# Kernel optimization log

Measured on AMD Instinct MI355X. Metric: run time of the kernel, lower is better.

The kernel has to match this reference:

```python
import jax, jax.numpy as jnp
import numpy as np

P, T, UNITS = 256, 65536, 128
WIDTH = 1.0


def setup_inputs() -> dict:
    key = jax.random.key(0)
    k1, k2, k3 = jax.random.split(key, 3)
    inputs = jax.random.normal(k1, (P, T), dtype=jnp.float32)
    player_weights = jax.random.normal(k2, (P,), dtype=jnp.float32)
    kernel = jax.random.normal(k3, (T, UNITS), dtype=jnp.float32) * 0.01
    bias = jnp.zeros((UNITS,), dtype=jnp.float32)
    state = jnp.zeros((P,), dtype=jnp.float32)
    return {"inputs": inputs, "player_weights": player_weights,
            "kernel": kernel, "bias": bias, "state": state}


def _phi(x):
    # Phi(x) = max(x,0) + min(x+width,0)
    return jnp.maximum(x, 0.0) + jnp.minimum(x + WIDTH, 0.0)


def _play_scan(x_seq, s0):
    # sequential play-operator recurrence: s_t = Phi(w*x_t - s_{t-1}) + s_{t-1}
    def step(s, x):
        s_new = _phi(x - s) + s
        return s_new, s_new
    _, ys = jax.lax.scan(step, s0, x_seq)
    return ys  # [T]


def reference(inputs, player_weights, kernel, bias, state):
    scaled = inputs * player_weights[:, None]          # [P, T]
    outs = jax.vmap(_play_scan)(scaled, state)         # [P, T]
    y = outs @ kernel + bias                           # [P, units]
    return jnp.tanh(y)
```

## Files before the change

### kernel.cpp

```cpp
#include <hip/hip_runtime.h>
#include <math.h>

#define Pn 256
#define Tn 65536
#define Un 128
#define NC 256
#define CHUNK 256
#define ST 32

typedef float f4 __attribute__((ext_vector_type(4)));

__global__ __launch_bounds__(1024) void kA(const float* __restrict__ in,
                                           const float* __restrict__ pw,
                                           float* __restrict__ Aarr,
                                           float* __restrict__ Barr) {
  __shared__ float As[4][Pn], Bs[4][Pn];
  const int c = blockIdx.x, tid = threadIdx.x;
  const int q = tid >> 8, p = tid & 255;
  const float w = pw[p];
  const f4* src = (const f4*)(in + (size_t)p * Tn + c * CHUNK + q * 64);
  float A = -3.402823466e38f, B = 3.402823466e38f;
#pragma unroll
  for (int i = 0; i < 16; ++i) {
    f4 v = src[i];
#pragma unroll
    for (int j = 0; j < 4; ++j) {
      float x = v[j] * w;
      A = fmaxf(A, x);
      B = fminf(fmaxf(B, x), x + 1.0f);
    }
  }
  As[q][p] = A;
  Bs[q][p] = B;
  __syncthreads();
  if (tid < Pn) {
    float Ac = As[0][tid], Bc = Bs[0][tid];
#pragma unroll
    for (int qq = 1; qq < 4; ++qq) {
      float a2 = As[qq][tid], b2 = Bs[qq][tid];
      Bc = fminf(fmaxf(Bc, a2), b2);
      Ac = fmaxf(Ac, a2);
    }
    Aarr[c * Pn + tid] = Ac;
    Barr[c * Pn + tid] = Bc;
  }
}

__global__ __launch_bounds__(256) void kB(const float* __restrict__ Aarr,
                                          const float* __restrict__ Barr,
                                          const float* __restrict__ st,
                                          float* __restrict__ sinb) {
  const int p = threadIdx.x;
  float s = st[p];
  for (int c = 0; c < NC; ++c) {
    sinb[c * Pn + p] = s;
    s = fminf(fmaxf(s, Aarr[c * Pn + p]), Barr[c * Pn + p]);
  }
}

template <bool ATOMIC>
__global__ __launch_bounds__(256, 1) void kC(const float* __restrict__ in,
                                             const float* __restrict__ pw,
                                             const float* __restrict__ Kg,
                                             const float* __restrict__ sinb,
                                             float* __restrict__ outp) {
  __shared__ float sS[ST][Pn];
  __shared__ float sK[ST][Un];
  const int c = blockIdx.x, tid = threadIdx.x;

  const float w = pw[tid];
  float s = sinb[c * Pn + tid];
  const f4* src = (const f4*)(in + (size_t)tid * Tn + c * CHUNK);

  const int ug = tid & 7, pg = tid >> 3;
  const int p0 = pg * 8;
  float acc[8][16];
#pragma unroll
  for (int a = 0; a < 8; ++a)
#pragma unroll
    for (int b = 0; b < 16; ++b) acc[a][b] = 0.0f;

  const f4* Kt = (const f4*)(Kg + (size_t)c * CHUNK * Un);

  for (int sub = 0; sub < CHUNK / ST; ++sub) {
#pragma unroll
    for (int k = 0; k < 4; ++k) {
      int idx = k * 256 + tid;
      int r = idx >> 5, col = idx & 31;
      *(f4*)&sK[r][col * 4] = Kt[(size_t)(sub * ST + r) * (Un / 4) + col];
    }
#pragma unroll
    for (int i4 = 0; i4 < ST / 4; ++i4) {
      f4 v = src[sub * (ST / 4) + i4];
#pragma unroll
      for (int j = 0; j < 4; ++j) {
        float x = v[j] * w;
        s = fminf(fmaxf(s, x), x + 1.0f);
        sS[i4 * 4 + j][tid] = s;
      }
    }
    __syncthreads();
#pragma unroll 2
    for (int i = 0; i < ST; ++i) {
      f4 sv0 = *(const f4*)&sS[i][p0];
      f4 sv1 = *(const f4*)&sS[i][p0 + 4];
      f4 kv0 = *(const f4*)&sK[i][ug * 4];
      f4 kv1 = *(const f4*)&sK[i][32 + ug * 4];
      f4 kv2 = *(const f4*)&sK[i][64 + ug * 4];
      f4 kv3 = *(const f4*)&sK[i][96 + ug * 4];
#pragma unroll
      for (int a = 0; a < 8; ++a) {
        float sa = (a < 4) ? sv0[a] : sv1[a - 4];
#pragma unroll
        for (int l = 0; l < 4; ++l) {
          acc[a][0 + l]  += sa * kv0[l];
          acc[a][4 + l]  += sa * kv1[l];
          acc[a][8 + l]  += sa * kv2[l];
          acc[a][12 + l] += sa * kv3[l];
        }
      }
    }
    __syncthreads();
  }

  if (ATOMIC) {
#pragma unroll
    for (int a = 0; a < 8; ++a)
#pragma unroll
      for (int k = 0; k < 4; ++k)
#pragma unroll
        for (int l = 0; l < 4; ++l)
          atomicAdd(&outp[(size_t)(p0 + a) * Un + k * 32 + ug * 4 + l],
                    acc[a][k * 4 + l]);
  } else {
    float* base = outp + (size_t)c * (Pn * Un);
#pragma unroll
    for (int a = 0; a < 8; ++a)
#pragma unroll
      for (int k = 0; k < 4; ++k) {
        f4 v;
#pragma unroll
        for (int l = 0; l < 4; ++l) v[l] = acc[a][k * 4 + l];
        *(f4*)&base[(size_t)(p0 + a) * Un + k * 32 + ug * 4] = v;
      }
  }
}

__global__ __launch_bounds__(256) void kD(const float* __restrict__ part,
                                          const float* __restrict__ bias,
                                          float* __restrict__ out) {
  const int g = blockIdx.x * 256 + threadIdx.x;
  const int u = g & (Un - 1);
  float a = 0.0f;
#pragma unroll 8
  for (int c = 0; c < NC; ++c) a += part[(size_t)c * (Pn * Un) + g];
  out[g] = tanhf(a + bias[u]);
}

__global__ __launch_bounds__(256) void kD2(float* __restrict__ out,
                                           const float* __restrict__ bias) {
  const int g = blockIdx.x * 256 + threadIdx.x;
  out[g] = tanhf(out[g] + bias[g & (Un - 1)]);
}

extern "C" void kernel_launch(void* const* d_in, const int* in_sizes, int n_in,
                              void* d_out, int out_size, void* d_ws,
                              size_t ws_size, hipStream_t stream) {
  const float* in   = (const float*)d_in[0];
  const float* pw   = (const float*)d_in[1];
  const float* Kg   = (const float*)d_in[2];
  const float* bias = (const float*)d_in[3];
  const float* st   = (const float*)d_in[4];
  float* out = (float*)d_out;
  float* ws = (float*)d_ws;

  float* Aarr = ws;
  float* Barr = ws + NC * Pn;
  float* sinb = ws + 2 * NC * Pn;
  float* part = ws + 262144;

  const size_t needPart =
      (262144 + (size_t)NC * Pn * Un) * sizeof(float);

  kA<<<NC, 1024, 0, stream>>>(in, pw, Aarr, Barr);
  kB<<<1, Pn, 0, stream>>>(Aarr, Barr, st, sinb);

  if (ws_size >= needPart) {
    kC<false><<<NC, 256, 0, stream>>>(in, pw, Kg, sinb, part);
    kD<<<(Pn * Un) / 256, 256, 0, stream>>>(part, bias, out);
  } else {
    hipMemsetAsync(d_out, 0, (size_t)Pn * Un * sizeof(float), stream);
    kC<true><<<NC, 256, 0, stream>>>(in, pw, Kg, sinb, out);
    kD2<<<(Pn * Un) / 256, 256, 0, stream>>>(out, bias);
  }
}
```

Measured before the change: 231.5 us.

## Halve chunk size, wave-reduce clamp summaries, parallelize carry scan, widen GEMM blocks

Chunks are cut from 256 to 128 steps, giving 512 chunks. kA now reduces each chunk's clamp summary with wave shuffles, one wave per (player, chunk). kB scans the carries in two levels using 1024 threads instead of one serial 256-thread loop. kC uses 512-thread blocks with a 4x2 by 4x2 register tile, where only half the threads run the recurrence. kD splits its partial sum over four thread groups. The aim is more parallelism and shorter serial chains, but it doubles the partial-sum buffer that kD must read.

```diff
diff --git a/kernel.cpp b/kernel.cpp
--- a/kernel.cpp
+++ b/kernel.cpp
@@ -4,119 +4,139 @@
 #define Pn 256
 #define Tn 65536
 #define Un 128
-#define NC 256
-#define CHUNK 256
+#define NC 512
+#define CHUNK 128
 #define ST 32
 
 typedef float f4 __attribute__((ext_vector_type(4)));
+typedef float f2 __attribute__((ext_vector_type(2)));
+
 
 __global__ __launch_bounds__(1024) void kA(const float* __restrict__ in,
                                            const float* __restrict__ pw,
-                                           float* __restrict__ Aarr,
-                                           float* __restrict__ Barr) {
-  __shared__ float As[4][Pn], Bs[4][Pn];
-  const int c = blockIdx.x, tid = threadIdx.x;
-  const int q = tid >> 8, p = tid & 255;
+                                           f2* __restrict__ AB) {
+  const int tid = threadIdx.x;
+  const int W = blockIdx.x * 16 + (tid >> 6);
+  const int l = tid & 63;
+  const int c = W & (NC - 1);
+  const int p = W >> 9;
   const float w = pw[p];
-  const f4* src = (const f4*)(in + (size_t)p * Tn + c * CHUNK + q * 64);
+  f2 v = *(const f2*)(in + (size_t)p * Tn + (size_t)c * CHUNK + 2 * l);
+  const float x0 = v.x * w, x1 = v.y * w;
+  float A = fmaxf(x0, x1);
+  float B = fminf(fmaxf(x0 + 1.0f, x1), x1 + 1.0f);
+#pragma unroll
+  for (int off = 1; off < 64; off <<= 1) {
+    float A2 = __shfl_down(A, off);
+    float B2 = __shfl_down(B, off);
+    B = fminf(fmaxf(B, A2), B2);
+    A = fmaxf(A, A2);
+  }
+  if (l == 0) {
+    f2 r; r.x = A; r.y = B;
+    AB[(size_t)c * Pn + p] = r;
+  }
+}
+
+__global__ __launch_bounds__(1024) void kB(const f2* __restrict__ AB,
+                                           const float* __restrict__ st,
+                                           float* __restrict__ sinb) {
+  __shared__ float qA[4][Pn], qB[4][Pn], sq[4][Pn];
+  const int p = threadIdx.x & 255, q = threadIdx.x >> 8;
+  const int c0 = q * (NC / 4);
   float A = -3.402823466e38f, B = 3.402823466e38f;
-#pragma unroll
-  for (int i = 0; i < 16; ++i) {
-    f4 v = src[i];
-#pragma unroll
-    for (int j = 0; j < 4; ++j) {
-      float x = v[j] * w;
-      A = fmaxf(A, x);
-      B = fminf(fmaxf(B, x), x + 1.0f);
-    }
-  }
-  As[q][p] = A;
-  Bs[q][p] = B;
+  for (int j = 0; j < NC / 4; ++j) {
+    f2 ab = AB[(size_t)(c0 + j) * Pn + p];
+    B = fminf(fmaxf(B, ab.x), ab.y);
+    A = fmaxf(A, ab.x);
+  }
+  qA[q][p] = A;
+  qB[q][p] = B;
   __syncthreads();
-  if (tid < Pn) {
-    float Ac = As[0][tid], Bc = Bs[0][tid];
-#pragma unroll
-    for (int qq = 1; qq < 4; ++qq) {
-      float a2 = As[qq][tid], b2 = Bs[qq][tid];
-      Bc = fminf(fmaxf(Bc, a2), b2);
-      Ac = fmaxf(Ac, a2);
-    }
-    Aarr[c * Pn + tid] = Ac;
-    Barr[c * Pn + tid] = Bc;
-  }
-}
-
-__global__ __launch_bounds__(256) void kB(const float* __restrict__ Aarr,
-                                          const float* __restrict__ Barr,
-                                          const float* __restrict__ st,
-                                          float* __restrict__ sinb) {
-  const int p = threadIdx.x;
-  float s = st[p];
-  for (int c = 0; c < NC; ++c) {
-    sinb[c * Pn + p] = s;
-    s = fminf(fmaxf(s, Aarr[c * Pn + p]), Barr[c * Pn + p]);
-  }
-}
-
-template <bool ATOMIC>
-__global__ __launch_bounds__(256, 1) void kC(const float* __restrict__ in,
+  if (threadIdx.x < Pn) {
+    float s = st[p];
+#pragma unroll
+    for (int qq = 0; qq < 4; ++qq) {
+      sq[qq][p] = s;
+      s = fminf(fmaxf(s, qA[qq][p]), qB[qq][p]);
+    }
+  }
+  __syncthreads();
+  float s = sq[q][p];
+  for (int j = 0; j < NC / 4; ++j) {
+    sinb[(size_t)(c0 + j) * Pn + p] = s;
+    f2 ab = AB[(size_t)(c0 + j) * Pn + p];
+    s = fminf(fmaxf(s, ab.x), ab.y);
+  }
+}
+
+template <int CPG, bool ATOMIC>
+__global__ __launch_bounds__(512, 4) void kC(const float* __restrict__ in,
                                              const float* __restrict__ pw,
                                              const float* __restrict__ Kg,
                                              const float* __restrict__ sinb,
                                              float* __restrict__ outp) {
   __shared__ float sS[ST][Pn];
   __shared__ float sK[ST][Un];
-  const int c = blockIdx.x, tid = threadIdx.x;
-
-  const float w = pw[tid];
-  float s = sinb[c * Pn + tid];
-  const f4* src = (const f4*)(in + (size_t)tid * Tn + c * CHUNK);
-
-  const int ug = tid & 7, pg = tid >> 3;
-  const int p0 = pg * 8;
-  float acc[8][16];
-#pragma unroll
-  for (int a = 0; a < 8; ++a)
-#pragma unroll
-    for (int b = 0; b < 16; ++b) acc[a][b] = 0.0f;
-
-  const f4* Kt = (const f4*)(Kg + (size_t)c * CHUNK * Un);
-
-  for (int sub = 0; sub < CHUNK / ST; ++sub) {
-#pragma unroll
-    for (int k = 0; k < 4; ++k) {
-      int idx = k * 256 + tid;
+  const int tid = threadIdx.x;
+  const int c0 = blockIdx.x * CPG;
+
+  float w = 0.0f, s = 0.0f;
+  const f4* src = nullptr;
+  if (tid < Pn) {
+    w = pw[tid];
+    s = sinb[(size_t)c0 * Pn + tid];
+    src = (const f4*)(in + (size_t)tid * Tn + (size_t)c0 * CHUNK);
+  }
+
+  const int ug = tid & 15, pg = tid >> 4;
+  float acc[2][4][2][4];
+#pragma unroll
+  for (int k1 = 0; k1 < 2; ++k1)
+#pragma unroll
+    for (int a = 0; a < 4; ++a)
+#pragma unroll
+      for (int k2 = 0; k2 < 2; ++k2)
+#pragma unroll
+        for (int l = 0; l < 4; ++l) acc[k1][a][k2][l] = 0.0f;
+
+  const int nsub = (CHUNK * CPG) / ST;
+  for (int sub = 0; sub < nsub; ++sub) {
+    const f4* Kt = (const f4*)(Kg + ((size_t)c0 * CHUNK + sub * ST) * Un);
+#pragma unroll
+    for (int k = 0; k < 2; ++k) {
+      int idx = k * 512 + tid;
       int r = idx >> 5, col = idx & 31;
-      *(f4*)&sK[r][col * 4] = Kt[(size_t)(sub * ST + r) * (Un / 4) + col];
-    }
-#pragma unroll
-    for (int i4 = 0; i4 < ST / 4; ++i4) {
-      f4 v = src[sub * (ST / 4) + i4];
-#pragma unroll
-      for (int j = 0; j < 4; ++j) {
-        float x = v[j] * w;
-        s = fminf(fmaxf(s, x), x + 1.0f);
-        sS[i4 * 4 + j][tid] = s;
+      *(f4*)&sK[r][col * 4] = Kt[r * 32 + col];
+    }
+    if (tid < Pn) {
+#pragma unroll
+      for (int i4 = 0; i4 < ST / 4; ++i4) {
+        f4 v = src[sub * (ST / 4) + i4];
+#pragma unroll
+        for (int j = 0; j < 4; ++j) {
+          float x = v[j] * w;
+          s = fminf(fmaxf(s, x), x + 1.0f);
+          sS[i4 * 4 + j][tid] = s;
+        }
       }
     }
     __syncthreads();
 #pragma unroll 2
     for (int i = 0; i < ST; ++i) {
-      f4 sv0 = *(const f4*)&sS[i][p0];
-      f4 sv1 = *(const f4*)&sS[i][p0 + 4];
+      f4 sv0 = *(const f4*)&sS[i][pg * 4];
+      f4 sv1 = *(const f4*)&sS[i][128 + pg * 4];
       f4 kv0 = *(const f4*)&sK[i][ug * 4];
-      f4 kv1 = *(const f4*)&sK[i][32 + ug * 4];
-      f4 kv2 = *(const f4*)&sK[i][64 + ug * 4];
-      f4 kv3 = *(const f4*)&sK[i][96 + ug * 4];
-#pragma unroll
-      for (int a = 0; a < 8; ++a) {
-        float sa = (a < 4) ? sv0[a] : sv1[a - 4];
+      f4 kv1 = *(const f4*)&sK[i][64 + ug * 4];
+#pragma unroll
+      for (int a = 0; a < 4; ++a) {
+        float s0 = sv0[a], s1 = sv1[a];
 #pragma unroll
         for (int l = 0; l < 4; ++l) {
-          acc[a][0 + l]  += sa * kv0[l];
-          acc[a][4 + l]  += sa * kv1[l];
-          acc[a][8 + l]  += sa * kv2[l];
-          acc[a][12 + l] += sa * kv3[l];
+          acc[0][a][0][l] += s0 * kv0[l];
+          acc[0][a][1][l] += s0 * kv1[l];
+          acc[1][a][0][l] += s1 * kv0[l];
+          acc[1][a][1][l] += s1 * kv1[l];
         }
       }
     }
@@ -125,36 +145,53 @@
 
   if (ATOMIC) {
 #pragma unroll
-    for (int a = 0; a < 8; ++a)
-#pragma unroll
-      for (int k = 0; k < 4; ++k)
-#pragma unroll
-        for (int l = 0; l < 4; ++l)
-          atomicAdd(&outp[(size_t)(p0 + a) * Un + k * 32 + ug * 4 + l],
-                    acc[a][k * 4 + l]);
+    for (int k1 = 0; k1 < 2; ++k1)
+#pragma unroll
+      for (int a = 0; a < 4; ++a) {
+        int pp = k1 * 128 + pg * 4 + a;
+#pragma unroll
+        for (int k2 = 0; k2 < 2; ++k2)
+#pragma unroll
+          for (int l = 0; l < 4; ++l)
+            atomicAdd(&outp[(size_t)pp * Un + k2 * 64 + ug * 4 + l],
+                      acc[k1][a][k2][l]);
+      }
   } else {
-    float* base = outp + (size_t)c * (Pn * Un);
-#pragma unroll
-    for (int a = 0; a < 8; ++a)
-#pragma unroll
-      for (int k = 0; k < 4; ++k) {
-        f4 v;
-#pragma unroll
-        for (int l = 0; l < 4; ++l) v[l] = acc[a][k * 4 + l];
-        *(f4*)&base[(size_t)(p0 + a) * Un + k * 32 + ug * 4] = v;
-      }
-  }
-}
-
+    float* base = outp + (size_t)blockIdx.x * (Pn * Un);
+#pragma unroll
+    for (int k1 = 0; k1 < 2; ++k1)
+#pragma unroll
+      for (int a = 0; a < 4; ++a) {
+        int pp = k1 * 128 + pg * 4 + a;
+#pragma unroll
+        for (int k2 = 0; k2 < 2; ++k2) {
+          f4 v;
+#pragma unroll
+          for (int l = 0; l < 4; ++l) v[l] = acc[k1][a][k2][l];
+          *(f4*)&base[(size_t)pp * Un + k2 * 64 + ug * 4] = v;
+        }
+      }
+  }
+}
+
+template <int NP>
 __global__ __launch_bounds__(256) void kD(const float* __restrict__ part,
                                           const float* __restrict__ bias,
                                           float* __restrict__ out) {
-  const int g = blockIdx.x * 256 + threadIdx.x;
-  const int u = g & (Un - 1);
+  __shared__ float red[4][64];
+  const int tid = threadIdx.x;
+  const int o = tid & 63, qc = tid >> 6;
+  const int g = blockIdx.x * 64 + o;
   float a = 0.0f;
-#pragma unroll 8
-  for (int c = 0; c < NC; ++c) a += part[(size_t)c * (Pn * Un) + g];
-  out[g] = tanhf(a + bias[u]);
+#pragma unroll 4
+  for (int k = 0; k < NP / 4; ++k)
+    a += part[(size_t)(qc + 4 * k) * (Pn * Un) + g];
+  red[qc][o] = a;
+  __syncthreads();
+  if (tid < 64) {
+    float t = red[0][o] + red[1][o] + red[2][o] + red[3][o];
+    out[g] = tanhf(t + bias[g & (Un - 1)]);
+  }
 }
 
 __global__ __launch_bounds__(256) void kD2(float* __restrict__ out,
@@ -172,25 +209,28 @@
   const float* bias = (const float*)d_in[3];
   const float* st   = (const float*)d_in[4];
   float* out = (float*)d_out;
-  float* ws = (float*)d_ws;
-
-  float* Aarr = ws;
-  float* Barr = ws + NC * Pn;
-  float* sinb = ws + 2 * NC * Pn;
-  float* part = ws + 262144;
-
-  const size_t needPart =
-      (262144 + (size_t)NC * Pn * Un) * sizeof(float);
-
-  kA<<<NC, 1024, 0, stream>>>(in, pw, Aarr, Barr);
-  kB<<<1, Pn, 0, stream>>>(Aarr, Barr, st, sinb);
-
-  if (ws_size >= needPart) {
-    kC<false><<<NC, 256, 0, stream>>>(in, pw, Kg, sinb, part);
-    kD<<<(Pn * Un) / 256, 256, 0, stream>>>(part, bias, out);
+  float* wsf = (float*)d_ws;
+
+  f2* AB      = (f2*)wsf;
+  float* sinb = wsf + 2 * NC * Pn;
+  float* part = wsf + 3 * NC * Pn;
+
+  const size_t base_f = (size_t)3 * NC * Pn;
+  const size_t need1 = (base_f + (size_t)NC * Pn * Un) * 4;
+  const size_t need2 = (base_f + (size_t)(NC / 2) * Pn * Un) * 4;
+
+  kA<<<(Pn * NC) / 16, 1024, 0, stream>>>(in, pw, AB);
+  kB<<<1, 1024, 0, stream>>>(AB, st, sinb);
+
+  if (ws_size >= need1) {
+    kC<1, false><<<NC, 512, 0, stream>>>(in, pw, Kg, sinb, part);
+    kD<NC><<<(Pn * Un) / 64, 256, 0, stream>>>(part, bias, out);
+  } else if (ws_size >= need2) {
+    kC<2, false><<<NC / 2, 512, 0, stream>>>(in, pw, Kg, sinb, part);
+    kD<NC / 2><<<(Pn * Un) / 64, 256, 0, stream>>>(part, bias, out);
   } else {
-    hipMemsetAsync(d_out, 0, (size_t)Pn * Un * sizeof(float), stream);
-    kC<true><<<NC, 256, 0, stream>>>(in, pw, Kg, sinb, out);
+    hipMemsetAsync(out, 0, (size_t)Pn * Un * sizeof(float), stream);
+    kC<2, true><<<NC / 2, 512, 0, stream>>>(in, pw, Kg, sinb, out);
     kD2<<<(Pn * Un) / 256, 256, 0, stream>>>(out, bias);
   }
 }
```

Result: no change. 234.9 us (+1.5%).
